# Kernel optimization log

Measured on AMD Instinct MI355X. Metric: run time of the kernel, lower is better.

## Reference

```python
import jax, jax.numpy as jnp
import numpy as np

B, N_SPINS, D_MODEL, K_MC = 256, 128, 768, 25


def setup_inputs() -> dict:
    key = jax.random.key(0)
    k1, k2, k3 = jax.random.split(key, 3)
    features = jax.random.normal(k1, (B, N_SPINS, D_MODEL), dtype=jnp.float32)
    coalitions = jax.random.randint(k2, (K_MC, N_SPINS), 0, 2, dtype=jnp.int32)
    w_v = jax.random.normal(k3, (D_MODEL, D_MODEL), dtype=jnp.float32) * 0.02
    scale = jnp.full((1,), 0.1, dtype=jnp.float32)
    return {"features": features, "coalitions": coalitions, "w_v": w_v, "scale": scale}


def reference(features, coalitions, w_v, scale):
    # features: [B, n, d]; coalitions: [K, n] in {0,1}; w_v: [d, d]; scale: [1]
    c = coalitions.astype(features.dtype)                      # [K, n]
    # coalition_value batched over all K coalitions at once:
    # sum_j mask[k,j] * features[b,j,:]  (sum and linear proj commute)
    s = jnp.einsum('kn,bnd->bkd', c, features)                 # [B, K, d]
    proj = s @ w_v                                             # [B, K, d]
    norm = jnp.linalg.norm(proj, axis=-1)                      # [B, K]
    cv = jax.nn.relu(norm * scale[0])                          # coalition values [B, K]
    # Shapley estimate: mean(v | i in S) - mean(v | i not in S)
    cnt_with = c.sum(axis=0)                                   # [n]
    cnt_without = c.shape[0] - cnt_with
    v_with = (cv @ c) / jnp.maximum(cnt_with, 1.0)             # [B, n]
    v_without = (cv @ (1.0 - c)) / jnp.maximum(cnt_without, 1.0)
    valid = (cnt_with > 0) & (cnt_without > 0)                 # [n]
    shapley = jnp.where(valid, v_with - v_without, 0.0)        # [B, n]
    return shapley
```

## Files before the change

kernel.cpp:

```cpp
#include <hip/hip_runtime.h>
#include <hip/hip_bf16.h>
#include <stdint.h>

#define NB  256
#define NSP 128
#define DM  768
#define KMC 25
#define MROWS (NB*KMC)

#define OFF_S    0u
#define OFF_WT   9830400u
#define OFF_N2   11010048u
#define OFF_COEF 11035648u

typedef __attribute__((ext_vector_type(8))) short bf16x8;
typedef __attribute__((ext_vector_type(4))) float f32x4;
typedef __attribute__((ext_vector_type(16))) float f32x16;
typedef unsigned int u32;

#define GLOAD_LDS16(gp, lp) \
  __builtin_amdgcn_global_load_lds((const __attribute__((address_space(1))) u32*)(gp), \
                                   (__attribute__((address_space(3))) u32*)(lp), 16, 0, 0)

#define KA_WAITV_BAR(N) asm volatile("s_waitcnt vmcnt(" #N ")\n\ts_barrier" ::: "memory")
#define KA_BAR()        asm volatile("s_barrier" ::: "memory")

#define KACH (16 * 384)

__global__ __launch_bounds__(256, 2) void kA_prep(const float* __restrict__ f,
                                                  const int* __restrict__ co,
                                                  const float* __restrict__ wv,
                                                  char* __restrict__ ws) {
  __shared__ __align__(16) char smem[3 * KACH * 4];
  const int bid = blockIdx.x;
  const int tid = threadIdx.x;

  if (bid >= 512) {
    const int blk = bid - 512;
    const int t = tid;
    if (blk < 144) {
      __hip_bfloat16 (*lt)[66] = (__hip_bfloat16(*)[66])smem;
      const int bi = blk / 12, bj = blk % 12;
      const int k0 = bi * 64, n0 = bj * 64;
      #pragma unroll
      for (int i = 0; i < 16; ++i) {
        int idx = t + i * 256;
        int r = idx >> 6, c = idx & 63;
        lt[c][r] = __float2bfloat16(wv[(size_t)(k0 + r) * DM + n0 + c]);
      }
      __syncthreads();
      __hip_bfloat16* wT = (__hip_bfloat16*)(ws + OFF_WT);
      #pragma unroll
      for (int i = 0; i < 16; ++i) {
        int idx = t + i * 256;
        int r = idx >> 6, c = idx & 63;
        wT[(size_t)(n0 + r) * DM + k0 + c] = lt[r][c];
      }
    } else if (blk == 144) {
      if (t < NSP) {
        const int n = t;
        int cw = 0;
        #pragma unroll
        for (int k = 0; k < KMC; ++k) cw += co[k * NSP + n];
        const int cwo = KMC - cw;
        const bool valid = (cw > 0) && (cwo > 0);
        float* coefT = (float*)(ws + OFF_COEF);
        #pragma unroll
        for (int k = 0; k < 28; ++k) {
          float v = 0.f;
          if (valid && k < KMC) v = co[k * NSP + n] ? (1.f / (float)cw) : (-1.f / (float)cwo);
          coefT[n * 28 + k] = v;
        }
      }
    } else {
      int i = (blk - 145) * 256 + t;
      if (i < MROWS) ((float*)(ws + OFF_N2))[i] = 0.f;
    }
    return;
  }

  const int b = bid >> 1;
  const int half = bid & 1;
  const int w = tid >> 6;
  const int lane = tid & 63;
  const int l31 = lane & 31, l5 = lane >> 5;

  float (*Fs)[KACH] = (float(*)[KACH])smem;
  __hip_bfloat16* s = (__hip_bfloat16*)(ws + OFF_S);

  bf16x8 Af[8];
  #pragma unroll
  for (int ks = 0; ks < 8; ++ks) {
    if (l31 < KMC) {
      const int* cp = co + l31 * NSP + ks * 16 + l5 * 8;
      int4 c0 = *(const int4*)(cp);
      int4 c1 = *(const int4*)(cp + 4);
      __hip_bfloat16 h;
      h = __float2bfloat16((float)c0.x); Af[ks][0] = *(short*)&h;
      h = __float2bfloat16((float)c0.y); Af[ks][1] = *(short*)&h;
      h = __float2bfloat16((float)c0.z); Af[ks][2] = *(short*)&h;
      h = __float2bfloat16((float)c0.w); Af[ks][3] = *(short*)&h;
      h = __float2bfloat16((float)c1.x); Af[ks][4] = *(short*)&h;
      h = __float2bfloat16((float)c1.y); Af[ks][5] = *(short*)&h;
      h = __float2bfloat16((float)c1.z); Af[ks][6] = *(short*)&h;
      h = __float2bfloat16((float)c1.w); Af[ks][7] = *(short*)&h;
    } else {
      #pragma unroll
      for (int j = 0; j < 8; ++j) Af[ks][j] = 0;
    }
  }
  asm volatile("s_waitcnt vmcnt(0)" ::: "memory");

  const float* fb = f + (size_t)b * NSP * DM + half * 384;
  int goff[6];
  #pragma unroll
  for (int q = 0; q < 6; ++q) {
    int e = (w * 6 + q) * 256 + lane * 4;
    int r = e / 384, c = e - r * 384;
    goff[q] = r * DM + c;
  }

  f32x16 ac[3];
  #pragma unroll
  for (int nt = 0; nt < 3; ++nt)
    #pragma unroll
    for (int r = 0; r < 16; ++r) ac[nt][r] = 0.f;

#define KA_ISSUE(ck, bi) { \
    const float* fp_ = fb + (size_t)(ck) * 16 * DM; \
    _Pragma("unroll") for (int q = 0; q < 6; ++q) \
      GLOAD_LDS16(fp_ + goff[q], (char*)&Fs[(bi)][0] + ((w * 6 + q) << 10)); }

#define KA_MFMA(ks, bi) { \
    _Pragma("unroll") for (int nt = 0; nt < 3; ++nt) { \
      bf16x8 Bf; \
      _Pragma("unroll") for (int j = 0; j < 8; ++j) { \
        float v_ = Fs[(bi)][(l5 * 8 + j) * 384 + w * 96 + nt * 32 + l31]; \
        __hip_bfloat16 h_ = __float2bfloat16(v_); \
        Bf[j] = *(short*)&h_; } \
      ac[nt] = __builtin_amdgcn_mfma_f32_32x32x16_bf16(Af[ks], Bf, ac[nt], 0, 0, 0); } }

  KA_ISSUE(0, 0) KA_ISSUE(1, 1) KA_ISSUE(2, 2)
  KA_WAITV_BAR(12);  KA_MFMA(0, 0)  KA_BAR();  KA_ISSUE(3, 0)
  KA_WAITV_BAR(12);  KA_MFMA(1, 1)  KA_BAR();  KA_ISSUE(4, 1)
  KA_WAITV_BAR(12);  KA_MFMA(2, 2)  KA_BAR();  KA_ISSUE(5, 2)
  KA_WAITV_BAR(12);  KA_MFMA(3, 0)  KA_BAR();  KA_ISSUE(6, 0)
  KA_WAITV_BAR(12);  KA_MFMA(4, 1)  KA_BAR();  KA_ISSUE(7, 1)
  KA_WAITV_BAR(12);  KA_MFMA(5, 2)
  KA_WAITV_BAR(6);   KA_MFMA(6, 0)
  KA_WAITV_BAR(0);   KA_MFMA(7, 1)

#undef KA_ISSUE
#undef KA_MFMA

  #pragma unroll
  for (int nt = 0; nt < 3; ++nt) {
    int dcol = half * 384 + w * 96 + nt * 32 + l31;
    #pragma unroll
    for (int r = 0; r < 16; ++r) {
      int row = (r & 3) + 8 * (r >> 2) + 4 * l5;
      if (row < KMC)
        s[((size_t)b * KMC + row) * DM + dcol] = __float2bfloat16(ac[nt][r]);
    }
  }
}

#define BM 64
#define BN 192
#define BK 32
#define NTK 24

__global__ __launch_bounds__(256) void kB(char* __restrict__ ws) {
  const int bid = blockIdx.x;
  const int tm = bid >> 2;
  const int tn = bid & 3;
  const int tid = threadIdx.x;
  const int wid = tid >> 6;
  const int lane = tid & 63;
  const int wm = wid >> 1;
  const int wn = wid & 1;

  const __hip_bfloat16* S  = (const __hip_bfloat16*)(ws + OFF_S);
  const __hip_bfloat16* WT = (const __hip_bfloat16*)(ws + OFF_WT);
  float* norm2 = (float*)(ws + OFF_N2);

  __shared__ __align__(16) char As[2][BM * BK * 2];
  __shared__ __align__(16) char Bs[2][BN * BK * 2];

  const char* gA; char *lAA0, *lAA1;
  {
    int li = wid * 64 + lane;
    int r = li >> 2, sl = li & 3;
    int slx = sl ^ ((r >> 1) & 3);
    gA = (const char*)(S + (size_t)(tm * BM + r) * DM) + slx * 16;
    lAA0 = As[0] + wid * 1024;
    lAA1 = As[1] + wid * 1024;
  }
  const char* gB[3]; char *lB0[3], *lB1[3];
  #pragma unroll
  for (int j = 0; j < 3; ++j) {
    int li = (wid * 3 + j) * 64 + lane;
    int r = li >> 2, sl = li & 3;
    int slx = sl ^ ((r >> 1) & 3);
    gB[j] = (const char*)(WT + (size_t)(tn * BN + r) * DM) + slx * 16;
    lB0[j] = Bs[0] + (wid * 3 + j) * 1024;
    lB1[j] = Bs[1] + (wid * 3 + j) * 1024;
  }

  auto stage = [&](int tk, int bsel) {
    size_t koff = (size_t)tk * (BK * 2);
    GLOAD_LDS16(gA + koff, bsel ? lAA1 : lAA0);
    #pragma unroll
    for (int j = 0; j < 3; ++j) GLOAD_LDS16(gB[j] + koff, bsel ? lB1[j] : lB0[j]);
  };

  f32x4 acc[2][6];
  #pragma unroll
  for (int m = 0; m < 2; ++m)
    #pragma unroll
    for (int n = 0; n < 6; ++n)
      #pragma unroll
      for (int j = 0; j < 4; ++j) acc[m][n][j] = 0.f;

  int offA[2], offB[6];
  #pragma unroll
  for (int m = 0; m < 2; ++m) {
    int r = wm * 32 + m * 16 + (lane & 15);
    int sl = (lane >> 4) ^ ((r >> 1) & 3);
    offA[m] = r * 64 + sl * 16;
  }
  #pragma unroll
  for (int n = 0; n < 6; ++n) {
    int r = wn * 96 + n * 16 + (lane & 15);
    int sl = (lane >> 4) ^ ((r >> 1) & 3);
    offB[n] = r * 64 + sl * 16;
  }

  stage(0, 0);
  for (int tk = 0; tk < NTK; ++tk) {
    int cur = tk & 1;
    __syncthreads();
    if (tk + 1 < NTK) stage(tk + 1, cur ^ 1);
    bf16x8 af[2], bfr[6];
    #pragma unroll
    for (int m = 0; m < 2; ++m) af[m] = *(const bf16x8*)(As[cur] + offA[m]);
    #pragma unroll
    for (int n = 0; n < 6; ++n) bfr[n] = *(const bf16x8*)(Bs[cur] + offB[n]);
    #pragma unroll
    for (int m = 0; m < 2; ++m)
      #pragma unroll
      for (int n = 0; n < 6; ++n)
        acc[m][n] = __builtin_amdgcn_mfma_f32_16x16x32_bf16(af[m], bfr[n], acc[m][n], 0, 0, 0);
  }

  float ps[2][4];
  #pragma unroll
  for (int m = 0; m < 2; ++m)
    #pragma unroll
    for (int i = 0; i < 4; ++i) {
      float v = 0.f;
      #pragma unroll
      for (int n = 0; n < 6; ++n) { float x = acc[m][n][i]; v += x * x; }
      #pragma unroll
      for (int d = 1; d < 16; d <<= 1) v += __shfl_xor(v, d, 64);
      ps[m][i] = v;
    }
  if ((lane & 15) == 0) {
    int g = lane >> 4;
    #pragma unroll
    for (int m = 0; m < 2; ++m)
      #pragma unroll
      for (int i = 0; i < 4; ++i)
        atomicAdd(&norm2[tm * BM + wm * 32 + m * 16 + g * 4 + i], ps[m][i]);
  }
}

__global__ __launch_bounds__(128) void kC(const char* __restrict__ ws,
                                          const float* __restrict__ scale,
                                          float* __restrict__ out) {
  const int b = blockIdx.x, n = threadIdx.x;
  const float* norm2 = (const float*)(ws + OFF_N2);
  const float* coefT = (const float*)(ws + OFF_COEF);
  __shared__ float cvs[32];
  if (n < KMC) {
    float nv = norm2[b * KMC + n];
    cvs[n] = fmaxf(sqrtf(fmaxf(nv, 0.f)) * scale[0], 0.f);
  } else if (n < 32) {
    cvs[n] = 0.f;
  }
  __syncthreads();
  float sum = 0.f;
  #pragma unroll
  for (int k = 0; k < KMC; ++k) sum += cvs[k] * coefT[n * 28 + k];
  out[b * NSP + n] = sum;
}

extern "C" void kernel_launch(void* const* d_in, const int* in_sizes, int n_in,
                              void* d_out, int out_size, void* d_ws, size_t ws_size,
                              hipStream_t stream) {
  const float* features   = (const float*)d_in[0];
  const int*   coalitions = (const int*)d_in[1];
  const float* wv         = (const float*)d_in[2];
  const float* scale      = (const float*)d_in[3];
  char* ws = (char*)d_ws;

  kA_prep<<<682, 256, 0, stream>>>(features, coalitions, wv, ws);
  kB<<<400, 256, 0, stream>>>(ws);
  kC<<<NB, 128, 0, stream>>>(ws, scale, (float*)d_out);
}
```

Measured before the change: 42.84 us.

## Fuse final Shapley reduction into GEMM via last-block counter and halve N tile

The kC launch is removed. The last kB block to finish, found through an atomic counter that kA resets, now computes coalition values and the Shapley output. The GEMM N tile also shrinks from 192 to 96, doubling the grid to 800 blocks for better CU occupancy. This saves one launch but makes a single block do all the epilogue work serially at the tail, and the smaller tile means A tiles are reloaded more often.

```diff
diff --git a/kernel.cpp b/kernel.cpp
--- a/kernel.cpp
+++ b/kernel.cpp
@@ -12,6 +12,7 @@
 #define OFF_WT   9830400u
 #define OFF_N2   11010048u
 #define OFF_COEF 11035648u
+#define OFF_CNT  11049984u
 
 typedef __attribute__((ext_vector_type(8))) short bf16x8;
 typedef __attribute__((ext_vector_type(4))) float f32x4;
@@ -71,6 +72,8 @@
           if (valid && k < KMC) v = co[k * NSP + n] ? (1.f / (float)cw) : (-1.f / (float)cwo);
           coefT[n * 28 + k] = v;
         }
+      } else if (t == NSP) {
+        *(u32*)(ws + OFF_CNT) = 0;
       }
     } else {
       int i = (blk - 145) * 256 + t;
@@ -166,14 +169,19 @@
 }
 
 #define BM 64
-#define BN 192
+#define BN 96
 #define BK 32
 #define NTK 24
-
-__global__ __launch_bounds__(256) void kB(char* __restrict__ ws) {
+#define KB_GRID 800
+#define KB_AOFF(bsel) ((bsel) * 4096)
+#define KB_BOFF(bsel) (8192 + (bsel) * 6144)
+
+__global__ __launch_bounds__(256) void kB(char* __restrict__ ws,
+                                          const float* __restrict__ scale,
+                                          float* __restrict__ out) {
   const int bid = blockIdx.x;
-  const int tm = bid >> 2;
-  const int tn = bid & 3;
+  const int tm = bid >> 3;
+  const int tn = bid & 7;
   const int tid = threadIdx.x;
   const int wid = tid >> 6;
   const int lane = tid & 63;
@@ -184,45 +192,44 @@
   const __hip_bfloat16* WT = (const __hip_bfloat16*)(ws + OFF_WT);
   float* norm2 = (float*)(ws + OFF_N2);
 
-  __shared__ __align__(16) char As[2][BM * BK * 2];
-  __shared__ __align__(16) char Bs[2][BN * BK * 2];
-
-  const char* gA; char *lAA0, *lAA1;
+  __shared__ __align__(16) char smemB[2 * 4096 + 2 * 6144];
+
+  const char* gA;
   {
     int li = wid * 64 + lane;
     int r = li >> 2, sl = li & 3;
     int slx = sl ^ ((r >> 1) & 3);
     gA = (const char*)(S + (size_t)(tm * BM + r) * DM) + slx * 16;
-    lAA0 = As[0] + wid * 1024;
-    lAA1 = As[1] + wid * 1024;
-  }
-  const char* gB[3]; char *lB0[3], *lB1[3];
-  #pragma unroll
-  for (int j = 0; j < 3; ++j) {
-    int li = (wid * 3 + j) * 64 + lane;
+  }
+  const char* gB0; const char* gB1;
+  {
+    int li = wid * 64 + lane;
     int r = li >> 2, sl = li & 3;
     int slx = sl ^ ((r >> 1) & 3);
-    gB[j] = (const char*)(WT + (size_t)(tn * BN + r) * DM) + slx * 16;
-    lB0[j] = Bs[0] + (wid * 3 + j) * 1024;
-    lB1[j] = Bs[1] + (wid * 3 + j) * 1024;
+    gB0 = (const char*)(WT + (size_t)(tn * BN + r) * DM) + slx * 16;
+    int j1 = (wid < 2) ? wid + 4 : wid;
+    int li1 = j1 * 64 + lane;
+    int r1 = li1 >> 2, sl1 = li1 & 3;
+    int slx1 = sl1 ^ ((r1 >> 1) & 3);
+    gB1 = (const char*)(WT + (size_t)(tn * BN + r1) * DM) + slx1 * 16;
   }
 
   auto stage = [&](int tk, int bsel) {
     size_t koff = (size_t)tk * (BK * 2);
-    GLOAD_LDS16(gA + koff, bsel ? lAA1 : lAA0);
-    #pragma unroll
-    for (int j = 0; j < 3; ++j) GLOAD_LDS16(gB[j] + koff, bsel ? lB1[j] : lB0[j]);
+    GLOAD_LDS16(gA + koff, smemB + KB_AOFF(bsel) + wid * 1024);
+    GLOAD_LDS16(gB0 + koff, smemB + KB_BOFF(bsel) + wid * 1024);
+    if (wid < 2) GLOAD_LDS16(gB1 + koff, smemB + KB_BOFF(bsel) + (wid + 4) * 1024);
   };
 
-  f32x4 acc[2][6];
+  f32x4 acc[2][3];
   #pragma unroll
   for (int m = 0; m < 2; ++m)
     #pragma unroll
-    for (int n = 0; n < 6; ++n)
+    for (int n = 0; n < 3; ++n)
       #pragma unroll
       for (int j = 0; j < 4; ++j) acc[m][n][j] = 0.f;
 
-  int offA[2], offB[6];
+  int offA[2], offB[3];
   #pragma unroll
   for (int m = 0; m < 2; ++m) {
     int r = wm * 32 + m * 16 + (lane & 15);
@@ -230,8 +237,8 @@
     offA[m] = r * 64 + sl * 16;
   }
   #pragma unroll
-  for (int n = 0; n < 6; ++n) {
-    int r = wn * 96 + n * 16 + (lane & 15);
+  for (int n = 0; n < 3; ++n) {
+    int r = wn * 48 + n * 16 + (lane & 15);
     int sl = (lane >> 4) ^ ((r >> 1) & 3);
     offB[n] = r * 64 + sl * 16;
   }
@@ -241,15 +248,17 @@
     int cur = tk & 1;
     __syncthreads();
     if (tk + 1 < NTK) stage(tk + 1, cur ^ 1);
-    bf16x8 af[2], bfr[6];
-    #pragma unroll
-    for (int m = 0; m < 2; ++m) af[m] = *(const bf16x8*)(As[cur] + offA[m]);
-    #pragma unroll
-    for (int n = 0; n < 6; ++n) bfr[n] = *(const bf16x8*)(Bs[cur] + offB[n]);
+    bf16x8 af[2], bfr[3];
     #pragma unroll
     for (int m = 0; m < 2; ++m)
-      #pragma unroll
-      for (int n = 0; n < 6; ++n)
+      af[m] = *(const bf16x8*)(smemB + KB_AOFF(cur) + offA[m]);
+    #pragma unroll
+    for (int n = 0; n < 3; ++n)
+      bfr[n] = *(const bf16x8*)(smemB + KB_BOFF(cur) + offB[n]);
+    #pragma unroll
+    for (int m = 0; m < 2; ++m)
+      #pragma unroll
+      for (int n = 0; n < 3; ++n)
         acc[m][n] = __builtin_amdgcn_mfma_f32_16x16x32_bf16(af[m], bfr[n], acc[m][n], 0, 0, 0);
   }
 
@@ -260,7 +269,7 @@
     for (int i = 0; i < 4; ++i) {
       float v = 0.f;
       #pragma unroll
-      for (int n = 0; n < 6; ++n) { float x = acc[m][n][i]; v += x * x; }
+      for (int n = 0; n < 3; ++n) { float x = acc[m][n][i]; v += x * x; }
       #pragma unroll
       for (int d = 1; d < 16; d <<= 1) v += __shfl_xor(v, d, 64);
       ps[m][i] = v;
@@ -273,26 +282,39 @@
       for (int i = 0; i < 4; ++i)
         atomicAdd(&norm2[tm * BM + wm * 32 + m * 16 + g * 4 + i], ps[m][i]);
   }
-}
-
-__global__ __launch_bounds__(128) void kC(const char* __restrict__ ws,
-                                          const float* __restrict__ scale,
-                                          float* __restrict__ out) {
-  const int b = blockIdx.x, n = threadIdx.x;
-  const float* norm2 = (const float*)(ws + OFF_N2);
+
+  __threadfence();
+  __syncthreads();
+  __shared__ int lastFlag;
+  if (tid == 0) {
+    u32 old = atomicAdd((u32*)(ws + OFF_CNT), 1u);
+    lastFlag = (old == KB_GRID - 1);
+  }
+  __syncthreads();
+  if (!lastFlag) return;
+  __threadfence();
+
   const float* coefT = (const float*)(ws + OFF_COEF);
-  __shared__ float cvs[32];
-  if (n < KMC) {
-    float nv = norm2[b * KMC + n];
-    cvs[n] = fmaxf(sqrtf(fmaxf(nv, 0.f)) * scale[0], 0.f);
-  } else if (n < 32) {
-    cvs[n] = 0.f;
-  }
-  __syncthreads();
-  float sum = 0.f;
-  #pragma unroll
-  for (int k = 0; k < KMC; ++k) sum += cvs[k] * coefT[n * 28 + k];
-  out[b * NSP + n] = sum;
+  float* cvLds = (float*)smemB;
+  const float scl = scale[0];
+  #pragma unroll
+  for (int p = 0; p < 2; ++p) {
+    __syncthreads();
+    for (int i = tid; i < 128 * KMC; i += 256) {
+      float nv = atomicAdd(&norm2[p * 128 * KMC + i], 0.0f);
+      cvLds[i] = fmaxf(sqrtf(fmaxf(nv, 0.f)) * scl, 0.f);
+    }
+    __syncthreads();
+    for (int idx = tid; idx < 128 * NSP; idx += 256) {
+      int bb = idx >> 7, n = idx & 127;
+      const float* cf = coefT + n * 28;
+      const float* cv = cvLds + bb * KMC;
+      float sum = 0.f;
+      #pragma unroll
+      for (int k = 0; k < KMC; ++k) sum += cv[k] * cf[k];
+      out[(size_t)(p * 128 + bb) * NSP + n] = sum;
+    }
+  }
 }
 
 extern "C" void kernel_launch(void* const* d_in, const int* in_sizes, int n_in,
@@ -305,6 +327,5 @@
   char* ws = (char*)d_ws;
 
   kA_prep<<<682, 256, 0, stream>>>(features, coalitions, wv, ws);
-  kB<<<400, 256, 0, stream>>>(ws);
-  kC<<<NB, 128, 0, stream>>>(ws, scale, (float*)d_out);
+  kB<<<KB_GRID, 256, 0, stream>>>(ws, scale, (float*)d_out);
 }
```

Result: slower. 156.6 us (+265.6%).
